# Kernel optimization log

Measured on AMD Instinct MI355X. Metric: run time of the kernel, lower is better.

## Reference

```python
import jax, jax.numpy as jnp
import numpy as np

I_OPP, H_OPP = 8, 50
N_GEN, H_GEN = 10, 10


def lstm_step(x, h, c, Wih, Whh, bih, bhh):
    # x: (I,), h,c: (H,), Wih: (4H,I), Whh: (4H,H) -- PyTorch gate order i,f,g,o
    gates = Wih @ x + bih + Whh @ h + bhh
    i, f, g, o = jnp.split(gates, 4)
    c2 = jax.nn.sigmoid(f) * c + jax.nn.sigmoid(i) * jnp.tanh(g)
    h2 = jax.nn.sigmoid(o) * jnp.tanh(c2)
    return h2, c2


def setup_inputs() -> dict:
    key = jax.random.key(0)
    ks = jax.random.split(key, 16)
    n = lambda k, s: jax.random.normal(k, s, dtype=jnp.float32) * 0.1
    return {
        "x": n(ks[0], (1, 1, I_OPP)),
        "h0_gen": n(ks[1], (N_GEN, H_GEN)),
        "c0_gen": n(ks[2], (N_GEN, H_GEN)),
        "W_ih_opp": n(ks[3], (4 * H_OPP, I_OPP)),
        "W_hh_opp": n(ks[4], (4 * H_OPP, H_OPP)),
        "b_ih_opp": n(ks[5], (4 * H_OPP,)),
        "b_hh_opp": n(ks[6], (4 * H_OPP,)),
        "W_ih_gen": n(ks[7], (N_GEN, 4 * H_GEN, I_OPP)),
        "W_hh_gen": n(ks[8], (N_GEN, 4 * H_GEN, H_GEN)),
        "b_ih_gen": n(ks[9], (N_GEN, 4 * H_GEN)),
        "b_hh_gen": n(ks[10], (N_GEN, 4 * H_GEN)),
        "W1": n(ks[11], (75, 150)),
        "b1": n(ks[12], (75,)),
        "W2": n(ks[13], (1, 75)),
        "b2": n(ks[14], (1,)),
    }


def reference(x, h0_gen, c0_gen, W_ih_opp, W_hh_opp, b_ih_opp, b_hh_opp,
              W_ih_gen, W_hh_gen, b_ih_gen, b_hh_gen, W1, b1, W2, b2):
    xv = x[0, 0]  # (8,) seq=1, batch=1
    # opp LSTM: source overwrites stateful result with a zero-initial-state call
    h_opp, _ = lstm_step(xv, jnp.zeros((H_OPP,), x.dtype), jnp.zeros((H_OPP,), x.dtype),
                         W_ih_opp, W_hh_opp, b_ih_opp, b_hh_opp)
    # 10 gen cells fused as one grouped gate computation
    gates = (jnp.einsum('gki,i->gk', W_ih_gen, xv) + b_ih_gen
             + jnp.einsum('gkh,gh->gk', W_hh_gen, h0_gen) + b_hh_gen)  # (10,40)
    i, f, g, o = jnp.split(gates, 4, axis=-1)
    c_gen = jax.nn.sigmoid(f) * c0_gen + jax.nn.sigmoid(i) * jnp.tanh(g)
    h_gen = jax.nn.sigmoid(o) * jnp.tanh(c_gen)  # (10,10)
    feat = jnp.concatenate([h_gen.reshape(-1), h_opp])  # (150,)
    out = W2 @ (W1 @ feat + b1) + b2  # no nonlinearity in source decode
    return out.reshape(1, 1, 1)
```

## Files before the change

kernel.cpp:

```cpp
#include <hip/hip_runtime.h>


__device__ __forceinline__ float fsigmoid(float v) {
    return 1.0f / (1.0f + __expf(-v));
}
__device__ __forceinline__ float ftanh(float v) {
    float e = __expf(2.0f * v);
    return (e - 1.0f) / (e + 1.0f);
}

__global__ __launch_bounds__(256) void net_kernel(
    const float* __restrict__ x,
    const float* __restrict__ h0_gen,
    const float* __restrict__ c0_gen,
    const float* __restrict__ W_ih_opp,
    const float* __restrict__ b_ih_opp,
    const float* __restrict__ b_hh_opp,
    const float* __restrict__ W_ih_gen,
    const float* __restrict__ W_hh_gen,
    const float* __restrict__ b_ih_gen,
    const float* __restrict__ b_hh_gen,
    const float* __restrict__ W1,
    const float* __restrict__ b1,
    const float* __restrict__ W2,
    const float* __restrict__ b2,
    float* __restrict__ out)
{
    __shared__ float xs[8];
    __shared__ float h0s[100];
    __shared__ float gates_opp[200];
    __shared__ float gates_gen[400];
    __shared__ float feat[150];
    __shared__ float part[150];

    const int t = threadIdx.x;

    if (t < 8)   xs[t]  = x[t];
    if (t < 100) h0s[t] = h0_gen[t];
    __syncthreads();

    if (t < 200) {
        float g = b_ih_opp[t] + b_hh_opp[t];
        #pragma unroll
        for (int k = 0; k < 8; ++k) g += W_ih_opp[t * 8 + k] * xs[k];
        gates_opp[t] = g;
    }
    for (int u = t; u < 400; u += 256) {
        float g = b_ih_gen[u] + b_hh_gen[u];
        #pragma unroll
        for (int k = 0; k < 8; ++k) g += W_ih_gen[u * 8 + k] * xs[k];
        const int cell = u / 40;
        #pragma unroll
        for (int h = 0; h < 10; ++h) g += W_hh_gen[u * 10 + h] * h0s[cell * 10 + h];
        gates_gen[u] = g;
    }
    __syncthreads();

    if (t < 100) {
        const int g = t / 10, j = t % 10;
        const int base = g * 40 + j;
        const float ig = fsigmoid(gates_gen[base]);
        const float fg = fsigmoid(gates_gen[base + 10]);
        const float gg = ftanh(gates_gen[base + 20]);
        const float og = fsigmoid(gates_gen[base + 30]);
        const float c  = fg * c0_gen[t] + ig * gg;
        feat[t] = og * ftanh(c);
    } else if (t >= 128 && t < 178) {
        const int j = t - 128;
        const float ig = fsigmoid(gates_opp[j]);
        const float gg = ftanh(gates_opp[100 + j]);
        const float og = fsigmoid(gates_opp[150 + j]);
        const float c  = ig * gg;
        feat[100 + j] = og * ftanh(c);
    }
    __syncthreads();

    if (t < 150) {
        const int r = t >> 1, half = t & 1;
        const float* wrow = W1 + r * 150 + half * 75;
        const float* frow = feat + half * 75;
        float s = 0.0f;
        #pragma unroll 5
        for (int k = 0; k < 75; ++k) s += wrow[k] * frow[k];
        part[t] = s;
    }
    __syncthreads();

    if (t < 64) {
        float s = 0.0f;
        for (int idx = t; idx < 75; idx += 64)
            s += W2[idx] * (part[2 * idx] + part[2 * idx + 1] + b1[idx]);
        #pragma unroll
        for (int off = 32; off > 0; off >>= 1)
            s += __shfl_down(s, off);
        if (t == 0) out[0] = s + b2[0];
    }
}

extern "C" void kernel_launch(void* const* d_in, const int* in_sizes, int n_in,
                              void* d_out, int out_size, void* d_ws, size_t ws_size,
                              hipStream_t stream) {
    const float* x        = (const float*)d_in[0];
    const float* h0_gen   = (const float*)d_in[1];
    const float* c0_gen   = (const float*)d_in[2];
    const float* W_ih_opp = (const float*)d_in[3];
    const float* b_ih_opp = (const float*)d_in[5];
    const float* b_hh_opp = (const float*)d_in[6];
    const float* W_ih_gen = (const float*)d_in[7];
    const float* W_hh_gen = (const float*)d_in[8];
    const float* b_ih_gen = (const float*)d_in[9];
    const float* b_hh_gen = (const float*)d_in[10];
    const float* W1       = (const float*)d_in[11];
    const float* b1       = (const float*)d_in[12];
    const float* W2       = (const float*)d_in[13];
    const float* b2       = (const float*)d_in[14];
    float* out = (float*)d_out;

    net_kernel<<<1, 256, 0, stream>>>(x, h0_gen, c0_gen,
                                      W_ih_opp, b_ih_opp, b_hh_opp,
                                      W_ih_gen, W_hh_gen, b_ih_gen, b_hh_gen,
                                      W1, b1, W2, b2, out);
}
```

Baseline: 9.832 us.

## Fuse gate computation with LSTM activations and split W1 rows three ways

```diff
diff --git a/kernel.cpp b/kernel.cpp
--- a/kernel.cpp
+++ b/kernel.cpp
@@ -26,70 +26,83 @@
     const float* __restrict__ b2,
     float* __restrict__ out)
 {
-    __shared__ float xs[8];
-    __shared__ float h0s[100];
-    __shared__ float gates_opp[200];
-    __shared__ float gates_gen[400];
-    __shared__ float feat[150];
-    __shared__ float part[150];
+    __shared__ float feat[152];
+    __shared__ float part[256];
 
     const int t = threadIdx.x;
 
-    if (t < 8)   xs[t]  = x[t];
-    if (t < 100) h0s[t] = h0_gen[t];
-    __syncthreads();
+    if (t < 100) {
+        const int cell = t / 10;
+        const int j = t - cell * 10;
 
-    if (t < 200) {
-        float g = b_ih_opp[t] + b_hh_opp[t];
+        const float4 x0 = ((const float4*)x)[0];
+        const float4 x1 = ((const float4*)x)[1];
+        const float xv[8] = {x0.x, x0.y, x0.z, x0.w, x1.x, x1.y, x1.z, x1.w};
+
+        float hv[10];
+        const float2* h2 = (const float2*)(h0_gen + cell * 10);
         #pragma unroll
-        for (int k = 0; k < 8; ++k) g += W_ih_opp[t * 8 + k] * xs[k];
-        gates_opp[t] = g;
-    }
-    for (int u = t; u < 400; u += 256) {
-        float g = b_ih_gen[u] + b_hh_gen[u];
+        for (int i = 0; i < 5; ++i) { float2 v = h2[i]; hv[2*i] = v.x; hv[2*i+1] = v.y; }
+
+        float gate[4];
         #pragma unroll
-        for (int k = 0; k < 8; ++k) g += W_ih_gen[u * 8 + k] * xs[k];
-        const int cell = u / 40;
+        for (int q = 0; q < 4; ++q) {
+            const int row = cell * 40 + q * 10 + j;
+            float g = b_ih_gen[row] + b_hh_gen[row];
+            const float4* wi = (const float4*)(W_ih_gen + row * 8);
+            const float4 a = wi[0], b = wi[1];
+            g += a.x*xv[0] + a.y*xv[1] + a.z*xv[2] + a.w*xv[3]
+               + b.x*xv[4] + b.y*xv[5] + b.z*xv[6] + b.w*xv[7];
+            const float2* wh = (const float2*)(W_hh_gen + row * 10);
+            #pragma unroll
+            for (int i = 0; i < 5; ++i) { float2 v = wh[i]; g += v.x*hv[2*i] + v.y*hv[2*i+1]; }
+            gate[q] = g;
+        }
+        const float c = fsigmoid(gate[1]) * c0_gen[t] + fsigmoid(gate[0]) * ftanh(gate[2]);
+        feat[t] = fsigmoid(gate[3]) * ftanh(c);
+    } else if (t >= 128 && t < 178) {
+        const int j = t - 128;
+
+        const float4 x0 = ((const float4*)x)[0];
+        const float4 x1 = ((const float4*)x)[1];
+        const float xv[8] = {x0.x, x0.y, x0.z, x0.w, x1.x, x1.y, x1.z, x1.w};
+
+        float gate[3];
+        const int rows[3] = {j, 100 + j, 150 + j};
         #pragma unroll
-        for (int h = 0; h < 10; ++h) g += W_hh_gen[u * 10 + h] * h0s[cell * 10 + h];
-        gates_gen[u] = g;
+        for (int q = 0; q < 3; ++q) {
+            const int row = rows[q];
+            float g = b_ih_opp[row] + b_hh_opp[row];
+            const float4* wi = (const float4*)(W_ih_opp + row * 8);
+            const float4 a = wi[0], b = wi[1];
+            g += a.x*xv[0] + a.y*xv[1] + a.z*xv[2] + a.w*xv[3]
+               + b.x*xv[4] + b.y*xv[5] + b.z*xv[6] + b.w*xv[7];
+            gate[q] = g;
+        }
+        const float c = fsigmoid(gate[0]) * ftanh(gate[1]);
+        feat[100 + j] = fsigmoid(gate[2]) * ftanh(c);
     }
     __syncthreads();
 
-    if (t < 100) {
-        const int g = t / 10, j = t % 10;
-        const int base = g * 40 + j;
-        const float ig = fsigmoid(gates_gen[base]);
-        const float fg = fsigmoid(gates_gen[base + 10]);
-        const float gg = ftanh(gates_gen[base + 20]);
-        const float og = fsigmoid(gates_gen[base + 30]);
-        const float c  = fg * c0_gen[t] + ig * gg;
-        feat[t] = og * ftanh(c);
-    } else if (t >= 128 && t < 178) {
-        const int j = t - 128;
-        const float ig = fsigmoid(gates_opp[j]);
-        const float gg = ftanh(gates_opp[100 + j]);
-        const float og = fsigmoid(gates_opp[150 + j]);
-        const float c  = ig * gg;
-        feat[100 + j] = og * ftanh(c);
-    }
-    __syncthreads();
-
-    if (t < 150) {
-        const int r = t >> 1, half = t & 1;
-        const float* wrow = W1 + r * 150 + half * 75;
-        const float* frow = feat + half * 75;
-        float s = 0.0f;
-        #pragma unroll 5
-        for (int k = 0; k < 75; ++k) s += wrow[k] * frow[k];
-        part[t] = s;
+    if (t < 225) {
+        const int r = t / 3;
+        const int c = t - r * 3;
+        const float2* wp = (const float2*)(W1 + r * 150 + c * 50);
+        const float2* fp = (const float2*)(feat + c * 50);
+        float s = (c == 0) ? b1[r] : 0.0f;
+        #pragma unroll
+        for (int i = 0; i < 25; ++i) {
+            const float2 wv = wp[i], fv = fp[i];
+            s += wv.x * fv.x + wv.y * fv.y;
+        }
+        part[t] = W2[r] * s;
+    } else {
+        part[t] = 0.0f;
     }
     __syncthreads();
 
     if (t < 64) {
-        float s = 0.0f;
-        for (int idx = t; idx < 75; idx += 64)
-            s += W2[idx] * (part[2 * idx] + part[2 * idx + 1] + b1[idx]);
+        float s = part[t] + part[t + 64] + part[t + 128] + part[t + 192];
         #pragma unroll
         for (int off = 32; off > 0; off >>= 1)
             s += __shfl_down(s, off);
```

Result: no change. 9.710 us (-1.2%).
